# Performance work log

Measured on AMD Instinct MI355X. Metric: run time of the kernel, lower is better.

Reference implementation:

```python
import jax, jax.numpy as jnp
import numpy as np


def _lin_relu(V, W, b):
    # LinearEmbedding: matmul + bias + ReLU (with_act_func=True default)
    return jax.nn.relu(jnp.matmul(V, W) + b)


def setup_inputs() -> dict:
    key = jax.random.key(0)
    ks = jax.random.split(key, 8)
    B, N, F = 4, 4096, 512
    C = F // 8
    sx = 1.0 / np.sqrt(F)
    return {
        "V": jax.random.normal(ks[0], (B, N, F), dtype=jnp.float32),
        "Wf": jax.random.normal(ks[1], (F, C), dtype=jnp.float32) * sx,
        "bf": jax.random.normal(ks[2], (C,), dtype=jnp.float32) * 5e-5 + 1e-4,
        "Wg": jax.random.normal(ks[3], (F, C), dtype=jnp.float32) * sx,
        "bg": jax.random.normal(ks[4], (C,), dtype=jnp.float32) * 5e-5 + 1e-4,
        "Wh": jax.random.normal(ks[5], (F, F), dtype=jnp.float32) * sx,
        "bh": jax.random.normal(ks[6], (F,), dtype=jnp.float32) * 5e-5 + 1e-4,
        "gamma": jax.random.normal(ks[7], (F,), dtype=jnp.float32),
    }


def reference(V, Wf, bf, Wg, bg, Wh, bh, gamma):
    f_out = _lin_relu(V, Wf, bf)          # [B, N, C]
    g_out = _lin_relu(V, Wg, bg)          # [B, N, C]
    h_out = _lin_relu(V, Wh, bh)          # [B, N, F]
    scores = jnp.einsum('bnc,bmc->bnm', f_out, g_out)  # [B, N, N]
    s = jax.nn.softmax(scores, axis=-1)
    o = jnp.einsum('bnm,bmf->bnf', s, h_out)            # [B, N, F]
    return gamma * o + V
```

## Files before the change

kernel.cpp:

```cpp
#include <hip/hip_runtime.h>
#include <hip/hip_bf16.h>
#include <math.h>

#define M_ROWS 16384
#define F_DIM 512
#define C_DIM 64

typedef short bf16x8 __attribute__((ext_vector_type(8)));
typedef float floatx4 __attribute__((ext_vector_type(4)));
typedef unsigned short ushortx8 __attribute__((ext_vector_type(8)));
typedef unsigned short ushortx4 __attribute__((ext_vector_type(4)));

static __device__ __forceinline__ unsigned short f2bf(float x) {
    __hip_bfloat16 h = __float2bfloat16(x);
    return *reinterpret_cast<unsigned short*>(&h);
}
static __device__ __forceinline__ float bf2f(unsigned short h) {
    unsigned int u = ((unsigned int)h) << 16;
    return __builtin_bit_cast(float, u);
}

static __device__ __forceinline__ void lgkm_barrier() {
    asm volatile("s_waitcnt lgkmcnt(0)\n\ts_barrier" ::: "memory");
}


__global__ __launch_bounds__(64) void prep_w_kernel(
    const float* __restrict__ Wf, const float* __restrict__ Wg,
    const float* __restrict__ Wh,
    unsigned short* __restrict__ wt_hi, unsigned short* __restrict__ wt_lo)
{
    const int c = blockIdx.x;
    const int t = threadIdx.x;
    const float* W; int ld, cl;
    if (c < 64)       { W = Wf; ld = C_DIM; cl = c; }
    else if (c < 128) { W = Wg; ld = C_DIM; cl = c - 64; }
    else              { W = Wh; ld = F_DIM; cl = c - 128; }
    const int ng = c >> 4, l16 = c & 15;
    for (int k = t; k < F_DIM; k += 64) {
        const float x = W[(size_t)k * ld + cl];
        const unsigned short h = f2bf(x);
        const int kh = k >> 5, qd = (k >> 3) & 3, j = k & 7;
        const size_t off = (((size_t)(ng * 16 + kh) * 64) + qd * 16 + l16) * 8 + j;
        wt_hi[off] = h;
        wt_lo[off] = f2bf(x - bf2f(h));
    }
}

#define BM 64
#define LDK 72

__global__ __launch_bounds__(256, 4) void embed_mfma_kernel(
    const float* __restrict__ V,
    const unsigned short* __restrict__ wt_hi, const unsigned short* __restrict__ wt_lo,
    const float* __restrict__ bf, const float* __restrict__ bg,
    const float* __restrict__ bh,
    unsigned short* __restrict__ f_bf, unsigned short* __restrict__ g_bf,
    unsigned short* __restrict__ h_sw)
{
    __shared__ __align__(16) unsigned short a_hi[BM][LDK];
    __shared__ __align__(16) unsigned short a_lo[BM][LDK];

    const int t  = threadIdx.x;
    const int R0 = blockIdx.x * BM;
    const bool fg = (blockIdx.y == 0);
    const int cbase = fg ? 0 : blockIdx.y * 128;

    const int w = t >> 6, lane = t & 63, quad = lane >> 4, l16 = lane & 15;

    floatx4 acc[4][2];
    #pragma unroll
    for (int rt = 0; rt < 4; ++rt)
        #pragma unroll
        for (int c = 0; c < 2; ++c)
            acc[rt][c] = (floatx4){0.f, 0.f, 0.f, 0.f};

    const int arow = t >> 4;
    const int acol = (t & 15) * 4;
    const int ng0  = (cbase >> 4) + w * 2;

    #pragma unroll 1
    for (int k0 = 0; k0 < F_DIM; k0 += 64) {
        lgkm_barrier();
        #pragma unroll
        for (int rr = 0; rr < 4; ++rr) {
            const int row = rr * 16 + arow;
            const float4 x = *(const float4*)(V + (size_t)(R0 + row) * F_DIM + k0 + acol);
            const float xs[4] = {x.x, x.y, x.z, x.w};
            ushortx4 hi, lo;
            #pragma unroll
            for (int jj = 0; jj < 4; ++jj) {
                const unsigned short hb2 = f2bf(xs[jj]);
                hi[jj] = hb2;
                lo[jj] = f2bf(xs[jj] - bf2f(hb2));
            }
            *(ushortx4*)&a_hi[row][acol] = hi;
            if (fg) *(ushortx4*)&a_lo[row][acol] = lo;
        }
        lgkm_barrier();
        #pragma unroll
        for (int kk = 0; kk < 2; ++kk) {
            const int kh = (k0 >> 5) + kk;
            const bf16x8 b0 = *(const bf16x8*)(wt_hi + (((size_t)(ng0 * 16 + kh)) * 64 + lane) * 8);
            const bf16x8 b1 = *(const bf16x8*)(wt_hi + (((size_t)((ng0 + 1) * 16 + kh)) * 64 + lane) * 8);
            bf16x8 ah[4];
            #pragma unroll
            for (int rt = 0; rt < 4; ++rt)
                ah[rt] = *(const bf16x8*)&a_hi[rt * 16 + l16][kk * 32 + quad * 8];
            #pragma unroll
            for (int rt = 0; rt < 4; ++rt) {
                acc[rt][0] = __builtin_amdgcn_mfma_f32_16x16x32_bf16(ah[rt], b0, acc[rt][0], 0, 0, 0);
                acc[rt][1] = __builtin_amdgcn_mfma_f32_16x16x32_bf16(ah[rt], b1, acc[rt][1], 0, 0, 0);
            }
            if (fg) {
                const bf16x8 c0 = *(const bf16x8*)(wt_lo + (((size_t)(ng0 * 16 + kh)) * 64 + lane) * 8);
                const bf16x8 c1 = *(const bf16x8*)(wt_lo + (((size_t)((ng0 + 1) * 16 + kh)) * 64 + lane) * 8);
                bf16x8 al[4];
                #pragma unroll
                for (int rt = 0; rt < 4; ++rt)
                    al[rt] = *(const bf16x8*)&a_lo[rt * 16 + l16][kk * 32 + quad * 8];
                #pragma unroll
                for (int rt = 0; rt < 4; ++rt) {
                    acc[rt][0] = __builtin_amdgcn_mfma_f32_16x16x32_bf16(ah[rt], c0, acc[rt][0], 0, 0, 0);
                    acc[rt][0] = __builtin_amdgcn_mfma_f32_16x16x32_bf16(al[rt], b0, acc[rt][0], 0, 0, 0);
                    acc[rt][1] = __builtin_amdgcn_mfma_f32_16x16x32_bf16(ah[rt], c1, acc[rt][1], 0, 0, 0);
                    acc[rt][1] = __builtin_amdgcn_mfma_f32_16x16x32_bf16(al[rt], b1, acc[rt][1], 0, 0, 0);
                }
            }
        }
    }

    #pragma unroll
    for (int rt = 0; rt < 4; ++rt) {
        #pragma unroll
        for (int c = 0; c < 2; ++c) {
            const int wtc  = cbase + w * 32 + c * 16 + l16;
            const int rowl = rt * 16 + quad * 4;
            const float bias = fg ? (wtc < 64 ? bf[wtc] : bg[wtc - 64]) : bh[wtc - 128];
            const floatx4 v = acc[rt][c];
            if (fg) {
                unsigned short* dst = (wtc < 64) ? (f_bf + wtc) : (g_bf + wtc - 64);
                #pragma unroll
                for (int r = 0; r < 4; ++r) {
                    const float z = v[r] + bias;
                    dst[(size_t)(R0 + rowl + r) * C_DIM] = f2bf(z > 0.f ? z : 0.f);
                }
            } else {
                const int hc   = wtc - 128;
                const int grow = R0 + rowl;
                const int b    = grow >> 12, rl = grow & 4095;
                const int T    = rl >> 6, mloc = rl & 63;
                const int kh2  = mloc >> 5, q2 = (mloc >> 3) & 3, j0 = mloc & 7;
                ushortx4 st;
                #pragma unroll
                for (int r = 0; r < 4; ++r) {
                    const float z = v[r] + bias;
                    st[r] = f2bf(z > 0.f ? z : 0.f);
                }
                const size_t off = ((((size_t)(b * 64 + T) * 64) + (hc >> 4) * 2 + kh2) * 64
                                    + q2 * 16 + (hc & 15)) * 8 + j0;
                *(ushortx4*)(h_sw + off) = st;
            }
        }
    }
}

#define QT 128
#define KT 64

__global__ __launch_bounds__(1024, 4) void attn_mfma_kernel(
    const unsigned short* __restrict__ f_bf, const unsigned short* __restrict__ g_bf,
    const unsigned short* __restrict__ h_sw, const float* __restrict__ gamma,
    const float* __restrict__ V, float* __restrict__ out)
{
    __shared__ __align__(16) unsigned short p_lds[2][QT * 64];
    __shared__ __align__(16) unsigned short g_lds[2][KT * 64];
    __shared__ float l_red[2][QT];
    __shared__ float l_inv[QT];

    const int t = threadIdx.x;
    const int w = t >> 6, lane = t & 63, quad = lane >> 4, l16 = lane & 15;
    const int sr = (w & 7) * 16, sc = (w >> 3) * 32;

    const int bid = blockIdx.x;
    const int b   = (bid & 7) >> 1;
    const int ch  = bid & 1;
    const int qb  = bid >> 3;
    const int R0  = qb * QT;

    const unsigned short* fb    = f_bf + ((size_t)b * 4096 + R0) * C_DIM;
    const unsigned short* gb    = g_bf + (size_t)b * 4096 * C_DIM;
    const unsigned short* hbase = h_sw + (size_t)b * 64 * 32768;
    const int hgrp = (ch * 16 + w) * 2;

    bf16x8 f0, f1;
    {
        const unsigned short* fr = fb + (size_t)(sr + l16) * C_DIM + quad * 8;
        f0 = *(const bf16x8*)fr;
        f1 = *(const bf16x8*)(fr + 32);
    }
    const float gam = gamma[ch * 256 + w * 16 + l16];

    floatx4 acc[8];
    #pragma unroll
    for (int rt = 0; rt < 8; ++rt)
        acc[rt] = (floatx4){0.f, 0.f, 0.f, 0.f};
    float run_l[4] = {0.f, 0.f, 0.f, 0.f};

    const int grow    = t >> 4, gk = (t & 15) * 4;
    const int g_swoff = grow * 128 + ((gk * 2) ^ ((grow & 7) << 4));
    ushortx4 greg = *(const ushortx4*)(gb + (size_t)grow * C_DIM + gk);

    const int sgrow0  = sc + l16;
    const int sgrow1  = sc + 16 + l16;
    const int sg0_off0 = sgrow0 * 128 + ((quad * 16)      ^ ((sgrow0 & 7) << 4));
    const int sg0_off1 = sgrow0 * 128 + ((quad * 16 + 64) ^ ((sgrow0 & 7) << 4));
    const int sg1_off0 = sgrow1 * 128 + ((quad * 16)      ^ ((sgrow1 & 7) << 4));
    const int sg1_off1 = sgrow1 * 128 + ((quad * 16 + 64) ^ ((sgrow1 & 7) << 4));

    for (int it = 0; it < 64; ++it) {
        const int buf = it & 1;
        const unsigned short* ht = hbase + (size_t)it * 32768 + (size_t)hgrp * 512;

        const bf16x8 h0 = *(const bf16x8*)(ht + (size_t)lane * 8);
        const bf16x8 h1 = *(const bf16x8*)(ht + 512 + (size_t)lane * 8);

        *(ushortx4*)((unsigned char*)&g_lds[buf][0] + g_swoff) = greg;
        if (it < 63)
            greg = *(const ushortx4*)(gb + (size_t)((it + 1) * KT + grow) * C_DIM + gk);
        lgkm_barrier();

        const unsigned char* gB = (const unsigned char*)&g_lds[buf][0];
        unsigned char*       pB = (unsigned char*)&p_lds[buf][0];

        {
            const bf16x8 ga0 = *(const bf16x8*)(gB + sg0_off0);
            const bf16x8 ga1 = *(const bf16x8*)(gB + sg0_off1);
            floatx4 cc = (floatx4){0.f, 0.f, 0.f, 0.f};
            cc = __builtin_amdgcn_mfma_f32_16x16x32_bf16(f0, ga0, cc, 0, 0, 0);
            cc = __builtin_amdgcn_mfma_f32_16x16x32_bf16(f1, ga1, cc, 0, 0, 0);
            const bf16x8 gb0 = *(const bf16x8*)(gB + sg1_off0);
            const bf16x8 gb1 = *(const bf16x8*)(gB + sg1_off1);
            floatx4 cd = (floatx4){0.f, 0.f, 0.f, 0.f};
            cd = __builtin_amdgcn_mfma_f32_16x16x32_bf16(f0, gb0, cd, 0, 0, 0);
            cd = __builtin_amdgcn_mfma_f32_16x16x32_bf16(f1, gb1, cd, 0, 0, 0);
            #pragma unroll
            for (int r = 0; r < 4; ++r) {
                const int prow = sr + quad * 4 + r;
                const int swp  = (prow & 7) << 4;
                const float p0 = __expf(cc[r] - 32.f);
                const float p1 = __expf(cd[r] - 32.f);
                run_l[r] += p0 + p1;
                *(unsigned short*)(pB + prow * 128 + (((sc + l16) * 2)      ^ swp)) = f2bf(p0);
                *(unsigned short*)(pB + prow * 128 + (((sc + 16 + l16) * 2) ^ swp)) = f2bf(p1);
            }
        }
        lgkm_barrier();

        #pragma unroll
        for (int rt = 0; rt < 8; ++rt) {
            const int prow = rt * 16 + l16;
            const int sw   = (prow & 7) << 4;
            const bf16x8 pf0 = *(const bf16x8*)(pB + prow * 128 + ((quad * 16)      ^ sw));
            const bf16x8 pf1 = *(const bf16x8*)(pB + prow * 128 + ((quad * 16 + 64) ^ sw));
            acc[rt] = __builtin_amdgcn_mfma_f32_16x16x32_bf16(pf0, h0, acc[rt], 0, 0, 0);
            acc[rt] = __builtin_amdgcn_mfma_f32_16x16x32_bf16(pf1, h1, acc[rt], 0, 0, 0);
        }
    }

    #pragma unroll
    for (int r = 0; r < 4; ++r) {
        float v = run_l[r];
        v += __shfl_xor(v, 1, 64);
        v += __shfl_xor(v, 2, 64);
        v += __shfl_xor(v, 4, 64);
        v += __shfl_xor(v, 8, 64);
        if (l16 == 0) l_red[w >> 3][sr + quad * 4 + r] = v;
    }
    __syncthreads();
    if (t < QT)
        l_inv[t] = 1.f / (l_red[0][t] + l_red[1][t]);
    __syncthreads();

    const float* Vb = V   + ((size_t)b * 4096 + R0) * F_DIM;
    float*       ob = out + ((size_t)b * 4096 + R0) * F_DIM;
    const int col = ch * 256 + w * 16 + l16;
    #pragma unroll
    for (int rt = 0; rt < 8; ++rt) {
        #pragma unroll
        for (int r = 0; r < 4; ++r) {
            const int row = rt * 16 + quad * 4 + r;
            ob[(size_t)row * F_DIM + col] =
                gam * acc[rt][r] * l_inv[row] + Vb[(size_t)row * F_DIM + col];
        }
    }
}

extern "C" void kernel_launch(void* const* d_in, const int* in_sizes, int n_in,
                              void* d_out, int out_size, void* d_ws, size_t ws_size,
                              hipStream_t stream) {
    const float* V     = (const float*)d_in[0];
    const float* Wf    = (const float*)d_in[1];
    const float* bf    = (const float*)d_in[2];
    const float* Wg    = (const float*)d_in[3];
    const float* bg    = (const float*)d_in[4];
    const float* Wh    = (const float*)d_in[5];
    const float* bh    = (const float*)d_in[6];
    const float* gamma = (const float*)d_in[7];
    float* out = (float*)d_out;

    unsigned short* f_bf  = (unsigned short*)d_ws;
    unsigned short* g_bf  = f_bf + (size_t)M_ROWS * C_DIM;
    unsigned short* h_sw  = g_bf + (size_t)M_ROWS * C_DIM;
    unsigned short* wt_hi = h_sw + (size_t)4 * F_DIM * 4096;
    unsigned short* wt_lo = wt_hi + (size_t)640 * F_DIM;

    prep_w_kernel<<<640, 64, 0, stream>>>(Wf, Wg, Wh, wt_hi, wt_lo);
    embed_mfma_kernel<<<dim3(M_ROWS / BM, 5), 256, 0, stream>>>(
        V, wt_hi, wt_lo, bf, bg, bh, f_bf, g_bf, h_sw);
    attn_mfma_kernel<<<256, 1024, 0, stream>>>(f_bf, g_bf, h_sw, gamma, V, out);
}
```

Before: 217.3 us.

## Retile attention PV stage to 64x32 per wave and remap embed grid for locality

In the attention kernel, each wave now covers 64 rows by 32 output columns instead of 128 rows by 16 columns. This halves the P-fragment LDS reads per wave, at the cost of twice as many global H loads per wave. Separately, the embed kernel moves from a 2D grid to a 1D grid of 1280 blocks. The new index mapping interleaves the five column-blocks of each group of eight row tiles, so blocks that read the same V rows run close together and can share L2/cache. The trade-off is more H register traffic in exchange for less LDS bandwidth pressure.

```diff
diff --git a/kernel.cpp b/kernel.cpp
--- a/kernel.cpp
+++ b/kernel.cpp
@@ -61,10 +61,13 @@
     __shared__ __align__(16) unsigned short a_hi[BM][LDK];
     __shared__ __align__(16) unsigned short a_lo[BM][LDK];
 
-    const int t  = threadIdx.x;
-    const int R0 = blockIdx.x * BM;
-    const bool fg = (blockIdx.y == 0);
-    const int cbase = fg ? 0 : blockIdx.y * 128;
+    const int t   = threadIdx.x;
+    const int bid = blockIdx.x;
+    const int yb  = (bid >> 3) % 5;
+    const int q   = (bid & 7) + 8 * ((bid >> 3) / 5);
+    const int R0  = q * BM;
+    const bool fg = (yb == 0);
+    const int cbase = fg ? 0 : yb * 128;
 
     const int w = t >> 6, lane = t & 63, quad = lane >> 4, l16 = lane & 15;
 
@@ -181,6 +184,7 @@
     const int t = threadIdx.x;
     const int w = t >> 6, lane = t & 63, quad = lane >> 4, l16 = lane & 15;
     const int sr = (w & 7) * 16, sc = (w >> 3) * 32;
+    const int rh = w >> 3, cw = w & 7;
 
     const int bid = blockIdx.x;
     const int b   = (bid & 7) >> 1;
@@ -191,7 +195,7 @@
     const unsigned short* fb    = f_bf + ((size_t)b * 4096 + R0) * C_DIM;
     const unsigned short* gb    = g_bf + (size_t)b * 4096 * C_DIM;
     const unsigned short* hbase = h_sw + (size_t)b * 64 * 32768;
-    const int hgrp = (ch * 16 + w) * 2;
+    const int hgrp = ch * 32 + cw * 4;
 
     bf16x8 f0, f1;
     {
@@ -199,12 +203,16 @@
         f0 = *(const bf16x8*)fr;
         f1 = *(const bf16x8*)(fr + 32);
     }
-    const float gam = gamma[ch * 256 + w * 16 + l16];
-
-    floatx4 acc[8];
-    #pragma unroll
-    for (int rt = 0; rt < 8; ++rt)
-        acc[rt] = (floatx4){0.f, 0.f, 0.f, 0.f};
+    float gam[2];
+    gam[0] = gamma[ch * 256 + cw * 32 + l16];
+    gam[1] = gamma[ch * 256 + cw * 32 + 16 + l16];
+
+    floatx4 acc[4][2];
+    #pragma unroll
+    for (int rt = 0; rt < 4; ++rt)
+        #pragma unroll
+        for (int c = 0; c < 2; ++c)
+            acc[rt][c] = (floatx4){0.f, 0.f, 0.f, 0.f};
     float run_l[4] = {0.f, 0.f, 0.f, 0.f};
 
     const int grow    = t >> 4, gk = (t & 15) * 4;
@@ -224,6 +232,8 @@
 
         const bf16x8 h0 = *(const bf16x8*)(ht + (size_t)lane * 8);
         const bf16x8 h1 = *(const bf16x8*)(ht + 512 + (size_t)lane * 8);
+        const bf16x8 h2 = *(const bf16x8*)(ht + 1024 + (size_t)lane * 8);
+        const bf16x8 h3 = *(const bf16x8*)(ht + 1536 + (size_t)lane * 8);
 
         *(ushortx4*)((unsigned char*)&g_lds[buf][0] + g_swoff) = greg;
         if (it < 63)
@@ -258,13 +268,15 @@
         lgkm_barrier();
 
         #pragma unroll
-        for (int rt = 0; rt < 8; ++rt) {
-            const int prow = rt * 16 + l16;
+        for (int rt = 0; rt < 4; ++rt) {
+            const int prow = rh * 64 + rt * 16 + l16;
             const int sw   = (prow & 7) << 4;
             const bf16x8 pf0 = *(const bf16x8*)(pB + prow * 128 + ((quad * 16)      ^ sw));
             const bf16x8 pf1 = *(const bf16x8*)(pB + prow * 128 + ((quad * 16 + 64) ^ sw));
-            acc[rt] = __builtin_amdgcn_mfma_f32_16x16x32_bf16(pf0, h0, acc[rt], 0, 0, 0);
-            acc[rt] = __builtin_amdgcn_mfma_f32_16x16x32_bf16(pf1, h1, acc[rt], 0, 0, 0);
+            acc[rt][0] = __builtin_amdgcn_mfma_f32_16x16x32_bf16(pf0, h0, acc[rt][0], 0, 0, 0);
+            acc[rt][0] = __builtin_amdgcn_mfma_f32_16x16x32_bf16(pf1, h1, acc[rt][0], 0, 0, 0);
+            acc[rt][1] = __builtin_amdgcn_mfma_f32_16x16x32_bf16(pf0, h2, acc[rt][1], 0, 0, 0);
+            acc[rt][1] = __builtin_amdgcn_mfma_f32_16x16x32_bf16(pf1, h3, acc[rt][1], 0, 0, 0);
         }
     }
 
@@ -284,14 +296,18 @@
 
     const float* Vb = V   + ((size_t)b * 4096 + R0) * F_DIM;
     float*       ob = out + ((size_t)b * 4096 + R0) * F_DIM;
-    const int col = ch * 256 + w * 16 + l16;
-    #pragma unroll
-    for (int rt = 0; rt < 8; ++rt) {
+    #pragma unroll
+    for (int rt = 0; rt < 4; ++rt) {
         #pragma unroll
         for (int r = 0; r < 4; ++r) {
-            const int row = rt * 16 + quad * 4 + r;
-            ob[(size_t)row * F_DIM + col] =
-                gam * acc[rt][r] * l_inv[row] + Vb[(size_t)row * F_DIM + col];
+            const int row = rh * 64 + rt * 16 + quad * 4 + r;
+            const float li = l_inv[row];
+            #pragma unroll
+            for (int c = 0; c < 2; ++c) {
+                const int col = ch * 256 + cw * 32 + c * 16 + l16;
+                ob[(size_t)row * F_DIM + col] =
+                    gam[c] * acc[rt][c][r] * li + Vb[(size_t)row * F_DIM + col];
+            }
         }
     }
 }
@@ -316,7 +332,7 @@
     unsigned short* wt_lo = wt_hi + (size_t)640 * F_DIM;
 
     prep_w_kernel<<<640, 64, 0, stream>>>(Wf, Wg, Wh, wt_hi, wt_lo);
-    embed_mfma_kernel<<<dim3(M_ROWS / BM, 5), 256, 0, stream>>>(
+    embed_mfma_kernel<<<1280, 256, 0, stream>>>(
         V, wt_hi, wt_lo, bf, bg, bh, f_bf, g_bf, h_sw);
     attn_mfma_kernel<<<256, 1024, 0, stream>>>(f_bf, g_bf, h_sw, gamma, V, out);
 }
```

Result: slower. 233.4 us (+7.4%).

## Pre-split V into MFMA-swizzled bf16 hi/lo buffers; double attention key tile

Applied to the files above, without the earlier changes.

A new kernel converts V once into bf16 hi/lo parts, stored in the MFMA fragment layout. The embedding GEMM then reads its A fragments straight from global memory, with no LDS staging or barriers, and stops redoing the fp32-to-bf16 split in each of the 5 column blocks. Separately, the attention kernel now processes 128 keys per iteration instead of 64, which halves the number of loop iterations and barriers and doubles the LDS used for P and G. The cost is an extra 32 MB write plus a re-read of the hi/lo V buffers, and higher LDS use, which may reduce occupancy.

```diff
diff --git a/kernel.cpp b/kernel.cpp
--- a/kernel.cpp
+++ b/kernel.cpp
@@ -47,26 +47,48 @@
     }
 }
 
+__global__ __launch_bounds__(256) void conv_v_kernel(
+    const float* __restrict__ V,
+    unsigned short* __restrict__ v_hi, unsigned short* __restrict__ v_lo)
+{
+    const int o   = blockIdx.x * 256 + threadIdx.x;
+    const int l16 = o & 15, kq = (o >> 4) & 3, kg = (o >> 6) & 15, rg = o >> 10;
+    const int row = rg * 16 + l16;
+    const int k   = kg * 32 + kq * 8;
+    const float4 x0 = *(const float4*)(V + (size_t)row * F_DIM + k);
+    const float4 x1 = *(const float4*)(V + (size_t)row * F_DIM + k + 4);
+    const float xs[8] = {x0.x, x0.y, x0.z, x0.w, x1.x, x1.y, x1.z, x1.w};
+    ushortx8 hi, lo;
+    #pragma unroll
+    for (int j = 0; j < 8; ++j) {
+        const unsigned short h = f2bf(xs[j]);
+        hi[j] = h;
+        lo[j] = f2bf(xs[j] - bf2f(h));
+    }
+    *(ushortx8*)(v_hi + (size_t)o * 8) = hi;
+    *(ushortx8*)(v_lo + (size_t)o * 8) = lo;
+}
+
 #define BM 64
-#define LDK 72
 
 __global__ __launch_bounds__(256, 4) void embed_mfma_kernel(
-    const float* __restrict__ V,
+    const unsigned short* __restrict__ v_hi, const unsigned short* __restrict__ v_lo,
     const unsigned short* __restrict__ wt_hi, const unsigned short* __restrict__ wt_lo,
     const float* __restrict__ bf, const float* __restrict__ bg,
     const float* __restrict__ bh,
     unsigned short* __restrict__ f_bf, unsigned short* __restrict__ g_bf,
     unsigned short* __restrict__ h_sw)
 {
-    __shared__ __align__(16) unsigned short a_hi[BM][LDK];
-    __shared__ __align__(16) unsigned short a_lo[BM][LDK];
-
     const int t  = threadIdx.x;
-    const int R0 = blockIdx.x * BM;
-    const bool fg = (blockIdx.y == 0);
-    const int cbase = fg ? 0 : blockIdx.y * 128;
+    const int q  = blockIdx.x;
+    const int yb = blockIdx.y;
+    const int R0 = q * BM;
+    const bool fg = (yb == 0);
+    const int cbase = fg ? 0 : yb * 128;
 
     const int w = t >> 6, lane = t & 63, quad = lane >> 4, l16 = lane & 15;
+    const int ng0 = (cbase >> 4) + w * 2;
+    const int rg0 = q * 4;
 
     floatx4 acc[4][2];
     #pragma unroll
@@ -75,57 +97,32 @@
         for (int c = 0; c < 2; ++c)
             acc[rt][c] = (floatx4){0.f, 0.f, 0.f, 0.f};
 
-    const int arow = t >> 4;
-    const int acol = (t & 15) * 4;
-    const int ng0  = (cbase >> 4) + w * 2;
-
-    #pragma unroll 1
-    for (int k0 = 0; k0 < F_DIM; k0 += 64) {
-        lgkm_barrier();
-        #pragma unroll
-        for (int rr = 0; rr < 4; ++rr) {
-            const int row = rr * 16 + arow;
-            const float4 x = *(const float4*)(V + (size_t)(R0 + row) * F_DIM + k0 + acol);
-            const float xs[4] = {x.x, x.y, x.z, x.w};
-            ushortx4 hi, lo;
-            #pragma unroll
-            for (int jj = 0; jj < 4; ++jj) {
-                const unsigned short hb2 = f2bf(xs[jj]);
-                hi[jj] = hb2;
-                lo[jj] = f2bf(xs[jj] - bf2f(hb2));
-            }
-            *(ushortx4*)&a_hi[row][acol] = hi;
-            if (fg) *(ushortx4*)&a_lo[row][acol] = lo;
-        }
-        lgkm_barrier();
-        #pragma unroll
-        for (int kk = 0; kk < 2; ++kk) {
-            const int kh = (k0 >> 5) + kk;
-            const bf16x8 b0 = *(const bf16x8*)(wt_hi + (((size_t)(ng0 * 16 + kh)) * 64 + lane) * 8);
-            const bf16x8 b1 = *(const bf16x8*)(wt_hi + (((size_t)((ng0 + 1) * 16 + kh)) * 64 + lane) * 8);
-            bf16x8 ah[4];
+    #pragma unroll 2
+    for (int kg = 0; kg < 16; ++kg) {
+        const bf16x8 b0 = *(const bf16x8*)(wt_hi + (((size_t)(ng0 * 16 + kg)) * 64 + lane) * 8);
+        const bf16x8 b1 = *(const bf16x8*)(wt_hi + (((size_t)((ng0 + 1) * 16 + kg)) * 64 + lane) * 8);
+        bf16x8 a[4];
+        #pragma unroll
+        for (int rt = 0; rt < 4; ++rt)
+            a[rt] = *(const bf16x8*)(v_hi + (((size_t)(rg0 + rt) * 16 + kg) * 64 + lane) * 8);
+        #pragma unroll
+        for (int rt = 0; rt < 4; ++rt) {
+            acc[rt][0] = __builtin_amdgcn_mfma_f32_16x16x32_bf16(a[rt], b0, acc[rt][0], 0, 0, 0);
+            acc[rt][1] = __builtin_amdgcn_mfma_f32_16x16x32_bf16(a[rt], b1, acc[rt][1], 0, 0, 0);
+        }
+        if (fg) {
+            const bf16x8 c0 = *(const bf16x8*)(wt_lo + (((size_t)(ng0 * 16 + kg)) * 64 + lane) * 8);
+            const bf16x8 c1 = *(const bf16x8*)(wt_lo + (((size_t)((ng0 + 1) * 16 + kg)) * 64 + lane) * 8);
+            bf16x8 al[4];
             #pragma unroll
             for (int rt = 0; rt < 4; ++rt)
-                ah[rt] = *(const bf16x8*)&a_hi[rt * 16 + l16][kk * 32 + quad * 8];
+                al[rt] = *(const bf16x8*)(v_lo + (((size_t)(rg0 + rt) * 16 + kg) * 64 + lane) * 8);
             #pragma unroll
             for (int rt = 0; rt < 4; ++rt) {
-                acc[rt][0] = __builtin_amdgcn_mfma_f32_16x16x32_bf16(ah[rt], b0, acc[rt][0], 0, 0, 0);
-                acc[rt][1] = __builtin_amdgcn_mfma_f32_16x16x32_bf16(ah[rt], b1, acc[rt][1], 0, 0, 0);
-            }
-            if (fg) {
-                const bf16x8 c0 = *(const bf16x8*)(wt_lo + (((size_t)(ng0 * 16 + kh)) * 64 + lane) * 8);
-                const bf16x8 c1 = *(const bf16x8*)(wt_lo + (((size_t)((ng0 + 1) * 16 + kh)) * 64 + lane) * 8);
-                bf16x8 al[4];
-                #pragma unroll
-                for (int rt = 0; rt < 4; ++rt)
-                    al[rt] = *(const bf16x8*)&a_lo[rt * 16 + l16][kk * 32 + quad * 8];
-                #pragma unroll
-                for (int rt = 0; rt < 4; ++rt) {
-                    acc[rt][0] = __builtin_amdgcn_mfma_f32_16x16x32_bf16(ah[rt], c0, acc[rt][0], 0, 0, 0);
-                    acc[rt][0] = __builtin_amdgcn_mfma_f32_16x16x32_bf16(al[rt], b0, acc[rt][0], 0, 0, 0);
-                    acc[rt][1] = __builtin_amdgcn_mfma_f32_16x16x32_bf16(ah[rt], c1, acc[rt][1], 0, 0, 0);
-                    acc[rt][1] = __builtin_amdgcn_mfma_f32_16x16x32_bf16(al[rt], b1, acc[rt][1], 0, 0, 0);
-                }
+                acc[rt][0] = __builtin_amdgcn_mfma_f32_16x16x32_bf16(a[rt],  c0, acc[rt][0], 0, 0, 0);
+                acc[rt][0] = __builtin_amdgcn_mfma_f32_16x16x32_bf16(al[rt], b0, acc[rt][0], 0, 0, 0);
+                acc[rt][1] = __builtin_amdgcn_mfma_f32_16x16x32_bf16(a[rt],  c1, acc[rt][1], 0, 0, 0);
+                acc[rt][1] = __builtin_amdgcn_mfma_f32_16x16x32_bf16(al[rt], b1, acc[rt][1], 0, 0, 0);
             }
         }
     }
@@ -166,15 +163,14 @@
 }
 
 #define QT 128
-#define KT 64
 
 __global__ __launch_bounds__(1024, 4) void attn_mfma_kernel(
     const unsigned short* __restrict__ f_bf, const unsigned short* __restrict__ g_bf,
     const unsigned short* __restrict__ h_sw, const float* __restrict__ gamma,
     const float* __restrict__ V, float* __restrict__ out)
 {
-    __shared__ __align__(16) unsigned short p_lds[2][QT * 64];
-    __shared__ __align__(16) unsigned short g_lds[2][KT * 64];
+    __shared__ __align__(16) unsigned short p_lds[2][QT * 128];
+    __shared__ __align__(16) unsigned short g_lds[2][128 * 64];
     __shared__ float l_red[2][QT];
     __shared__ float l_inv[QT];
 
@@ -207,52 +203,45 @@
         acc[rt] = (floatx4){0.f, 0.f, 0.f, 0.f};
     float run_l[4] = {0.f, 0.f, 0.f, 0.f};
 
-    const int grow    = t >> 4, gk = (t & 15) * 4;
-    const int g_swoff = grow * 128 + ((gk * 2) ^ ((grow & 7) << 4));
-    ushortx4 greg = *(const ushortx4*)(gb + (size_t)grow * C_DIM + gk);
-
-    const int sgrow0  = sc + l16;
-    const int sgrow1  = sc + 16 + l16;
-    const int sg0_off0 = sgrow0 * 128 + ((quad * 16)      ^ ((sgrow0 & 7) << 4));
-    const int sg0_off1 = sgrow0 * 128 + ((quad * 16 + 64) ^ ((sgrow0 & 7) << 4));
-    const int sg1_off0 = sgrow1 * 128 + ((quad * 16)      ^ ((sgrow1 & 7) << 4));
-    const int sg1_off1 = sgrow1 * 128 + ((quad * 16 + 64) ^ ((sgrow1 & 7) << 4));
-
-    for (int it = 0; it < 64; ++it) {
+    const int grow    = t >> 3, gc8 = (t & 7) * 8;
+    const int g_swoff = grow * 128 + ((gc8 * 2) ^ ((grow & 7) << 4));
+    ushortx8 greg = *(const ushortx8*)(gb + (size_t)grow * C_DIM + gc8);
+
+    for (int it = 0; it < 32; ++it) {
         const int buf = it & 1;
-        const unsigned short* ht = hbase + (size_t)it * 32768 + (size_t)hgrp * 512;
-
-        const bf16x8 h0 = *(const bf16x8*)(ht + (size_t)lane * 8);
-        const bf16x8 h1 = *(const bf16x8*)(ht + 512 + (size_t)lane * 8);
-
-        *(ushortx4*)((unsigned char*)&g_lds[buf][0] + g_swoff) = greg;
-        if (it < 63)
-            greg = *(const ushortx4*)(gb + (size_t)((it + 1) * KT + grow) * C_DIM + gk);
+
+        const unsigned short* ht0 = hbase + (size_t)(2 * it) * 32768 + (size_t)hgrp * 512;
+        const unsigned short* ht1 = ht0 + 32768;
+        const bf16x8 h0 = *(const bf16x8*)(ht0 + (size_t)lane * 8);
+        const bf16x8 h1 = *(const bf16x8*)(ht0 + 512 + (size_t)lane * 8);
+        const bf16x8 h2 = *(const bf16x8*)(ht1 + (size_t)lane * 8);
+        const bf16x8 h3 = *(const bf16x8*)(ht1 + 512 + (size_t)lane * 8);
+
+        *(ushortx8*)((unsigned char*)&g_lds[buf][0] + g_swoff) = greg;
+        if (it < 31)
+            greg = *(const ushortx8*)(gb + (size_t)((it + 1) * 128 + grow) * C_DIM + gc8);
         lgkm_barrier();
 
         const unsigned char* gB = (const unsigned char*)&g_lds[buf][0];
         unsigned char*       pB = (unsigned char*)&p_lds[buf][0];
 
-        {
-            const bf16x8 ga0 = *(const bf16x8*)(gB + sg0_off0);
-            const bf16x8 ga1 = *(const bf16x8*)(gB + sg0_off1);
+        #pragma unroll
+        for (int sct = 0; sct < 4; ++sct) {
+            const int s = sct >> 1, ct = sct & 1;
+            const int srow = s * 64 + sc + ct * 16 + l16;
+            const int sgw  = (srow & 7) << 4;
+            const bf16x8 g0 = *(const bf16x8*)(gB + srow * 128 + ((quad * 16)      ^ sgw));
+            const bf16x8 g1 = *(const bf16x8*)(gB + srow * 128 + ((quad * 16 + 64) ^ sgw));
             floatx4 cc = (floatx4){0.f, 0.f, 0.f, 0.f};
-            cc = __builtin_amdgcn_mfma_f32_16x16x32_bf16(f0, ga0, cc, 0, 0, 0);
-            cc = __builtin_amdgcn_mfma_f32_16x16x32_bf16(f1, ga1, cc, 0, 0, 0);
-            const bf16x8 gb0 = *(const bf16x8*)(gB + sg1_off0);
-            const bf16x8 gb1 = *(const bf16x8*)(gB + sg1_off1);
-            floatx4 cd = (floatx4){0.f, 0.f, 0.f, 0.f};
-            cd = __builtin_amdgcn_mfma_f32_16x16x32_bf16(f0, gb0, cd, 0, 0, 0);
-            cd = __builtin_amdgcn_mfma_f32_16x16x32_bf16(f1, gb1, cd, 0, 0, 0);
+            cc = __builtin_amdgcn_mfma_f32_16x16x32_bf16(f0, g0, cc, 0, 0, 0);
+            cc = __builtin_amdgcn_mfma_f32_16x16x32_bf16(f1, g1, cc, 0, 0, 0);
             #pragma unroll
             for (int r = 0; r < 4; ++r) {
+                const float p = __expf(cc[r] - 32.f);
+                run_l[r] += p;
                 const int prow = sr + quad * 4 + r;
-                const int swp  = (prow & 7) << 4;
-                const float p0 = __expf(cc[r] - 32.f);
-                const float p1 = __expf(cd[r] - 32.f);
-                run_l[r] += p0 + p1;
-                *(unsigned short*)(pB + prow * 128 + (((sc + l16) * 2)      ^ swp)) = f2bf(p0);
-                *(unsigned short*)(pB + prow * 128 + (((sc + 16 + l16) * 2) ^ swp)) = f2bf(p1);
+                const int bcol = (s * 64 + sc + ct * 16 + l16) * 2;
+                *(unsigned short*)(pB + prow * 256 + (bcol ^ ((prow & 7) << 4))) = f2bf(p);
             }
         }
         lgkm_barrier();
@@ -261,10 +250,15 @@
         for (int rt = 0; rt < 8; ++rt) {
             const int prow = rt * 16 + l16;
             const int sw   = (prow & 7) << 4;
-            const bf16x8 pf0 = *(const bf16x8*)(pB + prow * 128 + ((quad * 16)      ^ sw));
-            const bf16x8 pf1 = *(const bf16x8*)(pB + prow * 128 + ((quad * 16 + 64) ^ sw));
+            const unsigned char* pr = pB + prow * 256;
+            const bf16x8 pf0 = *(const bf16x8*)(pr + ((quad * 16)       ^ sw));
+            const bf16x8 pf1 = *(const bf16x8*)(pr + ((quad * 16 + 64)  ^ sw));
+            const bf16x8 pf2 = *(const bf16x8*)(pr + ((quad * 16 + 128) ^ sw));
+            const bf16x8 pf3 = *(const bf16x8*)(pr + ((quad * 16 + 192) ^ sw));
             acc[rt] = __builtin_amdgcn_mfma_f32_16x16x32_bf16(pf0, h0, acc[rt], 0, 0, 0);
             acc[rt] = __builtin_amdgcn_mfma_f32_16x16x32_bf16(pf1, h1, acc[rt], 0, 0, 0);
+            acc[rt] = __builtin_amdgcn_mfma_f32_16x16x32_bf16(pf2, h2, acc[rt], 0, 0, 0);
+            acc[rt] = __builtin_amdgcn_mfma_f32_16x16x32_bf16(pf3, h3, acc[rt], 0, 0, 0);
         }
     }
 
@@ -314,9 +308,12 @@
     unsigned short* h_sw  = g_bf + (size_t)M_ROWS * C_DIM;
     unsigned short* wt_hi = h_sw + (size_t)4 * F_DIM * 4096;
     unsigned short* wt_lo = wt_hi + (size_t)640 * F_DIM;
-
+    unsigned short* v_hi  = wt_lo + (size_t)640 * F_DIM;
+    unsigned short* v_lo  = v_hi + (size_t)M_ROWS * F_DIM;
+
+    conv_v_kernel<<<M_ROWS * F_DIM / 8 / 256, 256, 0, stream>>>(V, v_hi, v_lo);
     prep_w_kernel<<<640, 64, 0, stream>>>(Wf, Wg, Wh, wt_hi, wt_lo);
-    embed_mfma_kernel<<<dim3(M_ROWS / BM, 5), 256, 0, stream>>>(
-        V, wt_hi, wt_lo, bf, bg, bh, f_bf, g_bf, h_sw);
+    embed_mfma_kernel<<<dim3(256, 5), 256, 0, stream>>>(
+        v_hi, v_lo, wt_hi, wt_lo, bf, bg, bh, f_bf, g_bf, h_sw);
     attn_mfma_kernel<<<256, 1024, 0, stream>>>(f_bf, g_bf, h_sw, gamma, V, out);
 }
```

After: 247.0 us. +13.6%, slower.
